# Performance work log

Measured on AMD Instinct MI355X. Metric: run time of the kernel, lower is better.

Reference implementation:

```python
import jax, jax.numpy as jnp
import numpy as np

GS = 256      # grid/node count
PARAM = 128   # feature width
KC = 32       # keepconst (constant features)
I1, I2 = 64, 32
PK = PARAM - KC
K_DIV = 16.0  # neighbor-count normalizer
EPS = 1e-3    # Keras BatchNorm default epsilon
B = 4


def _bn(x, g, b, m, v):
    # inference-mode batch norm over last axis
    return (x - m) * jax.lax.rsqrt(v + EPS) * g + b


def setup_inputs() -> dict:
    key = jax.random.key(0)
    ks = jax.random.split(key, 24)
    mat = (jax.random.uniform(ks[0], (B, GS, GS)) < (K_DIV / GS)).astype(jnp.float32)
    val = jax.random.normal(ks[1], (B, GS, PARAM), dtype=jnp.float32)
    def w(k, shape):
        fan = shape[0] if len(shape) > 1 else shape[0]
        return jax.random.normal(k, shape, dtype=jnp.float32) * (1.0 / np.sqrt(fan))
    inp = {
        'mat': mat, 'val': val,
        'M1': w(ks[2], (2 * PARAM, I1)), 'B1': 0.05 * jax.random.normal(ks[3], (I1,)),
        'M2': w(ks[4], (I1, I2)),        'B2': 0.05 * jax.random.normal(ks[5], (I2,)),
        'M3': w(ks[6], (I2, PK)),        'B3': 0.05 * jax.random.normal(ks[7], (PK,)),
    }
    for idx, d in zip((1, 2, 3), (I1, I2, PK)):
        kk = jax.random.split(ks[7 + idx], 4)
        inp[f'g{idx}'] = 1.0 + 0.1 * jax.random.normal(kk[0], (d,), dtype=jnp.float32)
        inp[f'b{idx}'] = 0.1 * jax.random.normal(kk[1], (d,), dtype=jnp.float32)
        inp[f'm{idx}'] = 0.1 * jax.random.normal(kk[2], (d,), dtype=jnp.float32)
        inp[f'v{idx}'] = jax.random.uniform(kk[3], (d,), dtype=jnp.float32, minval=0.5, maxval=1.5)
    return inp


def reference(mat, val, M1, B1, M2, B2, M3, B3,
              g1, b1, m1, v1, g2, b2, m2, v2, g3, b3, m3, v3):
    con = val[:, :, :KC]
    # selector matmuls == gather: pair i -> (a=i//GS, b=i%GS)
    feat = jnp.repeat(val, GS, axis=1)          # (B, GS*GS, PARAM) = val_a
    vb = jnp.tile(val, (1, GS, 1))              # (B, GS*GS, PARAM) = val_b
    premlp = jnp.concatenate([feat, vb - feat], axis=-1)  # (B, GS*GS, 2*PARAM)
    s = jax.nn.relu(_bn(premlp @ M1 + B1, g1, b1, m1, v1))
    s = jax.nn.relu(_bn(s @ M2 + B2, g2, b2, m2, v2))
    s = jax.nn.relu(_bn(s @ M3 + B3, g3, b3, m3, v3))      # (B, GS*GS, PK)
    res = s.reshape(val.shape[0], GS, GS, PK)               # (B, a, b, PK)
    # masked scatter-sum over neighbor axis b
    summ = jnp.einsum('babk,bab->bak'.replace('a', 'x').replace('b', 'y', 1), res, mat) if False else \
        jnp.einsum('bxyk,bxy->bxk', res, mat)               # (B, GS, PK)
    var = jnp.clip(summ / K_DIV, -1.0, 1.0)                 # advrelu([-1,1]) == clip
    return jnp.concatenate([con, var], axis=-1)             # (B, GS, PARAM)
```

## Files before the change

kernel.cpp:

```cpp
#include <hip/hip_runtime.h>

#define GS    256
#define PARAM 128
#define KC    32
#define I1    64
#define I2    32
#define PK    96
#define B_    4
#define NROWS (B_ * GS)
#define EPS   1e-3f
#define KDIV_INV (1.0f / 16.0f)

constexpr int U_OFF   = 0;
constexpr int W_OFF   = NROWS * I1;
constexpr int M2F_OFF = 2 * NROWS * I1;
constexpr int C2_OFF  = M2F_OFF + I1 * I2;
constexpr int M3F_OFF = C2_OFF + I2;
constexpr int C3_OFF  = M3F_OFF + I2 * PK;
constexpr int C1_OFF  = C3_OFF + PK;

__device__ __forceinline__ float rdlane(float v, int l) {
    return __uint_as_float(__builtin_amdgcn_readlane(__float_as_uint(v), l));
}

__global__ __launch_bounds__(256) void glmlp_precompute(
    const float* __restrict__ val, const float* __restrict__ M1,
    const float* __restrict__ B1,
    const float* __restrict__ M2, const float* __restrict__ B2,
    const float* __restrict__ M3, const float* __restrict__ B3,
    const float* __restrict__ g1, const float* __restrict__ b1,
    const float* __restrict__ m1, const float* __restrict__ v1,
    const float* __restrict__ g2, const float* __restrict__ b2,
    const float* __restrict__ m2, const float* __restrict__ v2,
    const float* __restrict__ g3, const float* __restrict__ b3,
    const float* __restrict__ m3, const float* __restrict__ v3,
    float* __restrict__ ws, float* __restrict__ out)
{
    const int blk = blockIdx.x;
    const int t = threadIdx.x;

    if (blk < NROWS) {
        __shared__ float vrow[PARAM];
        __shared__ float red[4][I1];
        const int r = blk;
        if (t < PARAM) vrow[t] = val[r * PARAM + t];
        if (t < KC) out[r * PARAM + t] = val[r * PARAM + t];
        __syncthreads();

        const int i = t & (I1 - 1);
        const int q = t >> 6;
        const float* __restrict__ Mb = M1 + ((q >> 1) ? (PARAM * I1) : 0);
        const int p0 = (q & 1) * 64;
        float aa = 0.f, bb = 0.f;
        #pragma unroll 8
        for (int p = 0; p < 64; p += 2) {
            aa = fmaf(vrow[p0 + p],     Mb[(p0 + p) * I1 + i],     aa);
            bb = fmaf(vrow[p0 + p + 1], Mb[(p0 + p + 1) * I1 + i], bb);
        }
        red[q][i] = aa + bb;
        __syncthreads();

        if (q == 0) {
            const float T  = red[0][i] + red[1][i];
            const float Wv = red[2][i] + red[3][i];
            const float s1 = g1[i] * rsqrtf(v1[i] + EPS);
            ws[U_OFF + r * I1 + i] = (T - Wv) * s1;
            ws[W_OFF + r * I1 + i] = Wv * s1;
        }
    } else {
        if (t < I1) {
            const float s1 = g1[t] * rsqrtf(v1[t] + EPS);
            ws[C1_OFF + t] = B1[t] * s1 + b1[t] - m1[t] * s1;
        }
        if (t < I2) {
            const float s2 = g2[t] * rsqrtf(v2[t] + EPS);
            ws[C2_OFF + t] = B2[t] * s2 + b2[t] - m2[t] * s2;
        }
        if (t < PK) {
            const float s3 = g3[t] * rsqrtf(v3[t] + EPS);
            ws[C3_OFF + t] = B3[t] * s3 + b3[t] - m3[t] * s3;
        }
        for (int idx = t; idx < I1 * I2; idx += 256) {
            const int j = idx & (I2 - 1);
            const float s2 = g2[j] * rsqrtf(v2[j] + EPS);
            ws[M2F_OFF + idx] = M2[idx] * s2;
        }
        for (int idx = t; idx < I2 * PK; idx += 256) {
            const int k = idx % PK;
            const float s3 = g3[k] * rsqrtf(v3[k] + EPS);
            ws[M3F_OFF + idx] = M3[idx] * s3;
        }
    }
}

__global__ __launch_bounds__(256) void glmlp_pairs(
    const float* __restrict__ mat, const float* __restrict__ ws,
    float* __restrict__ out)
{
    const int t = threadIdx.x;
    const int lane = t & 63;
    const int r = blockIdx.x * 4 + (t >> 6);
    const int jj = lane & 31;
    const int wbase = r & ~(GS - 1);
    const float* __restrict__ W = ws + W_OFF;

    const unsigned long long bal0 = __ballot(mat[r * GS +   0 + lane] != 0.f);
    const unsigned long long bal1 = __ballot(mat[r * GS +  64 + lane] != 0.f);
    const unsigned long long bal2 = __ballot(mat[r * GS + 128 + lane] != 0.f);
    const unsigned long long bal3 = __ballot(mat[r * GS + 192 + lane] != 0.f);

    float m2col[I1];
    #pragma unroll
    for (int s = 0; s < I1; ++s)
        m2col[s] = ws[M2F_OFF + s * I2 + jj];
    float m3a[I2], m3b[I2];
    #pragma unroll
    for (int i = 0; i < I2; ++i) {
        m3a[i] = ws[M3F_OFF + i * PK + lane];
        m3b[i] = ws[M3F_OFF + i * PK + 64 + jj];
    }
    const float ux  = ws[U_OFF + r * I1 + lane] + ws[C1_OFF + lane];
    const float c2j = ws[C2_OFF + jj];
    const float c30 = ws[C3_OFF + lane];
    const float c31 = ws[C3_OFF + 64 + jj];

    unsigned long long cur = bal0;
    int c = 0;
    auto advance = [&]() -> int {
        while (cur == 0ULL) {
            ++c;
            if (c == 1)      cur = bal1;
            else if (c == 2) cur = bal2;
            else if (c == 3) cur = bal3;
            else             return -1;
        }
        const int b = __builtin_ctzll(cur);
        cur &= cur - 1;
        return (c << 6) + b;
    };

    float acc0 = 0.f, acc1 = 0.f;

    int y = advance();
    float wv = (y >= 0) ? W[(wbase + y) * I1 + lane] : 0.f;
    while (y >= 0) {
        const int yn = advance();
        const float wvn = (yn >= 0) ? W[(wbase + yn) * I1 + lane] : 0.f;

        const float h1 = fmaxf(ux + wv, 0.f);

        float a0 = 0.f, a1 = 0.f, a2 = 0.f, a3 = 0.f;
        #pragma unroll
        for (int s = 0; s < I1; s += 4) {
            a0 = fmaf(rdlane(h1, s + 0), m2col[s + 0], a0);
            a1 = fmaf(rdlane(h1, s + 1), m2col[s + 1], a1);
            a2 = fmaf(rdlane(h1, s + 2), m2col[s + 2], a2);
            a3 = fmaf(rdlane(h1, s + 3), m2col[s + 3], a3);
        }
        const float h2 = fmaxf((a0 + a1) + (a2 + a3) + c2j, 0.f);

        float d0a = c30, d0b = 0.f, d1a = c31, d1b = 0.f;
        #pragma unroll
        for (int i = 0; i < I2; i += 2) {
            const float he = rdlane(h2, i);
            const float ho = rdlane(h2, i + 1);
            d0a = fmaf(he, m3a[i],     d0a);
            d0b = fmaf(ho, m3a[i + 1], d0b);
            d1a = fmaf(he, m3b[i],     d1a);
            d1b = fmaf(ho, m3b[i + 1], d1b);
        }
        acc0 += fmaxf(d0a + d0b, 0.f);
        acc1 += fmaxf(d1a + d1b, 0.f);

        y = yn;
        wv = wvn;
    }

    {
        const float v0 = fminf(fmaxf(acc0 * KDIV_INV, -1.f), 1.f);
        out[r * PARAM + KC + lane] = v0;
        if (lane < 32) {
            const float v1 = fminf(fmaxf(acc1 * KDIV_INV, -1.f), 1.f);
            out[r * PARAM + KC + 64 + lane] = v1;
        }
    }
}

extern "C" void kernel_launch(void* const* d_in, const int* in_sizes, int n_in,
                              void* d_out, int out_size, void* d_ws, size_t ws_size,
                              hipStream_t stream) {
    const float* mat = (const float*)d_in[0];
    const float* val = (const float*)d_in[1];
    const float* M1  = (const float*)d_in[2];
    const float* B1  = (const float*)d_in[3];
    const float* M2  = (const float*)d_in[4];
    const float* B2  = (const float*)d_in[5];
    const float* M3  = (const float*)d_in[6];
    const float* B3  = (const float*)d_in[7];
    const float* g1  = (const float*)d_in[8];
    const float* b1  = (const float*)d_in[9];
    const float* m1  = (const float*)d_in[10];
    const float* v1  = (const float*)d_in[11];
    const float* g2  = (const float*)d_in[12];
    const float* b2  = (const float*)d_in[13];
    const float* m2  = (const float*)d_in[14];
    const float* v2  = (const float*)d_in[15];
    const float* g3  = (const float*)d_in[16];
    const float* b3  = (const float*)d_in[17];
    const float* m3  = (const float*)d_in[18];
    const float* v3  = (const float*)d_in[19];

    float* ws  = (float*)d_ws;
    float* out = (float*)d_out;

    hipLaunchKernelGGL(glmlp_precompute, dim3(NROWS + 1), dim3(256), 0, stream,
                       val, M1, B1, M2, B2, M3, B3,
                       g1, b1, m1, v1, g2, b2, m2, v2, g3, b3, m3, v3,
                       ws, out);

    hipLaunchKernelGGL(glmlp_pairs, dim3(NROWS / 4), dim3(256), 0, stream,
                       mat, ws, out);
}
```

Before: 122.5 us.

## Split each row's neighbors across four waves and fold BN constants into pairs kernel

The pairs kernel now assigns one block per row and has its four wavefronts stride through the row's neighbor list, then reduces their partial sums in shared memory. Previously each wave handled a whole row on its own, with 256 blocks. This raises parallelism from 256 to 1024 blocks, at the cost of a shared-memory reduction and a barrier. The folded BN weights and biases for layers 2 and 3 are now computed inside every block instead of in an extra precompute block, which adds redundant per-block loads and rsqrt work.

```diff
diff --git a/kernel.cpp b/kernel.cpp
--- a/kernel.cpp
+++ b/kernel.cpp
@@ -11,13 +11,8 @@
 #define EPS   1e-3f
 #define KDIV_INV (1.0f / 16.0f)
 
-constexpr int U_OFF   = 0;
-constexpr int W_OFF   = NROWS * I1;
-constexpr int M2F_OFF = 2 * NROWS * I1;
-constexpr int C2_OFF  = M2F_OFF + I1 * I2;
-constexpr int M3F_OFF = C2_OFF + I2;
-constexpr int C3_OFF  = M3F_OFF + I2 * PK;
-constexpr int C1_OFF  = C3_OFF + PK;
+constexpr int U_OFF = 0;
+constexpr int W_OFF = NROWS * I1;
 
 __device__ __forceinline__ float rdlane(float v, int l) {
     return __uint_as_float(__builtin_amdgcn_readlane(__float_as_uint(v), l));
@@ -25,81 +20,59 @@
 
 __global__ __launch_bounds__(256) void glmlp_precompute(
     const float* __restrict__ val, const float* __restrict__ M1,
-    const float* __restrict__ B1,
+    const float* __restrict__ g1, const float* __restrict__ v1,
+    float* __restrict__ ws, float* __restrict__ out)
+{
+    __shared__ float vrow[PARAM];
+    __shared__ float red[4][I1];
+    const int r = blockIdx.x;
+    const int t = threadIdx.x;
+
+    if (t < PARAM) vrow[t] = val[r * PARAM + t];
+    if (t < KC) out[r * PARAM + t] = val[r * PARAM + t];
+    __syncthreads();
+
+    const int i = t & (I1 - 1);
+    const int q = t >> 6;
+    const float* __restrict__ Mb = M1 + ((q >> 1) ? (PARAM * I1) : 0);
+    const int p0 = (q & 1) * 64;
+    float aa = 0.f, bb = 0.f;
+    #pragma unroll 8
+    for (int p = 0; p < 64; p += 2) {
+        aa = fmaf(vrow[p0 + p],     Mb[(p0 + p) * I1 + i],     aa);
+        bb = fmaf(vrow[p0 + p + 1], Mb[(p0 + p + 1) * I1 + i], bb);
+    }
+    red[q][i] = aa + bb;
+    __syncthreads();
+
+    if (q == 0) {
+        const float T  = red[0][i] + red[1][i];
+        const float Wv = red[2][i] + red[3][i];
+        const float s1 = g1[i] * rsqrtf(v1[i] + EPS);
+        ws[U_OFF + r * I1 + i] = (T - Wv) * s1;
+        ws[W_OFF + r * I1 + i] = Wv * s1;
+    }
+}
+
+__global__ __launch_bounds__(256) void glmlp_pairs(
+    const float* __restrict__ mat, const float* __restrict__ ws,
     const float* __restrict__ M2, const float* __restrict__ B2,
     const float* __restrict__ M3, const float* __restrict__ B3,
-    const float* __restrict__ g1, const float* __restrict__ b1,
-    const float* __restrict__ m1, const float* __restrict__ v1,
+    const float* __restrict__ B1, const float* __restrict__ g1,
+    const float* __restrict__ b1, const float* __restrict__ m1,
+    const float* __restrict__ v1,
     const float* __restrict__ g2, const float* __restrict__ b2,
     const float* __restrict__ m2, const float* __restrict__ v2,
     const float* __restrict__ g3, const float* __restrict__ b3,
     const float* __restrict__ m3, const float* __restrict__ v3,
-    float* __restrict__ ws, float* __restrict__ out)
-{
-    const int blk = blockIdx.x;
-    const int t = threadIdx.x;
-
-    if (blk < NROWS) {
-        __shared__ float vrow[PARAM];
-        __shared__ float red[4][I1];
-        const int r = blk;
-        if (t < PARAM) vrow[t] = val[r * PARAM + t];
-        if (t < KC) out[r * PARAM + t] = val[r * PARAM + t];
-        __syncthreads();
-
-        const int i = t & (I1 - 1);
-        const int q = t >> 6;
-        const float* __restrict__ Mb = M1 + ((q >> 1) ? (PARAM * I1) : 0);
-        const int p0 = (q & 1) * 64;
-        float aa = 0.f, bb = 0.f;
-        #pragma unroll 8
-        for (int p = 0; p < 64; p += 2) {
-            aa = fmaf(vrow[p0 + p],     Mb[(p0 + p) * I1 + i],     aa);
-            bb = fmaf(vrow[p0 + p + 1], Mb[(p0 + p + 1) * I1 + i], bb);
-        }
-        red[q][i] = aa + bb;
-        __syncthreads();
-
-        if (q == 0) {
-            const float T  = red[0][i] + red[1][i];
-            const float Wv = red[2][i] + red[3][i];
-            const float s1 = g1[i] * rsqrtf(v1[i] + EPS);
-            ws[U_OFF + r * I1 + i] = (T - Wv) * s1;
-            ws[W_OFF + r * I1 + i] = Wv * s1;
-        }
-    } else {
-        if (t < I1) {
-            const float s1 = g1[t] * rsqrtf(v1[t] + EPS);
-            ws[C1_OFF + t] = B1[t] * s1 + b1[t] - m1[t] * s1;
-        }
-        if (t < I2) {
-            const float s2 = g2[t] * rsqrtf(v2[t] + EPS);
-            ws[C2_OFF + t] = B2[t] * s2 + b2[t] - m2[t] * s2;
-        }
-        if (t < PK) {
-            const float s3 = g3[t] * rsqrtf(v3[t] + EPS);
-            ws[C3_OFF + t] = B3[t] * s3 + b3[t] - m3[t] * s3;
-        }
-        for (int idx = t; idx < I1 * I2; idx += 256) {
-            const int j = idx & (I2 - 1);
-            const float s2 = g2[j] * rsqrtf(v2[j] + EPS);
-            ws[M2F_OFF + idx] = M2[idx] * s2;
-        }
-        for (int idx = t; idx < I2 * PK; idx += 256) {
-            const int k = idx % PK;
-            const float s3 = g3[k] * rsqrtf(v3[k] + EPS);
-            ws[M3F_OFF + idx] = M3[idx] * s3;
-        }
-    }
-}
-
-__global__ __launch_bounds__(256) void glmlp_pairs(
-    const float* __restrict__ mat, const float* __restrict__ ws,
     float* __restrict__ out)
 {
+    __shared__ float partial[4][PK];
+
     const int t = threadIdx.x;
     const int lane = t & 63;
-    const int r = blockIdx.x * 4 + (t >> 6);
+    const int w = t >> 6;
+    const int r = blockIdx.x;
     const int jj = lane & 31;
     const int wbase = r & ~(GS - 1);
     const float* __restrict__ W = ws + W_OFF;
@@ -109,20 +82,27 @@
     const unsigned long long bal2 = __ballot(mat[r * GS + 128 + lane] != 0.f);
     const unsigned long long bal3 = __ballot(mat[r * GS + 192 + lane] != 0.f);
 
+    const float s2j = g2[jj] * rsqrtf(v2[jj] + EPS);
     float m2col[I1];
     #pragma unroll
     for (int s = 0; s < I1; ++s)
-        m2col[s] = ws[M2F_OFF + s * I2 + jj];
+        m2col[s] = M2[s * I2 + jj] * s2j;
+    const float c2j = (B2[jj] - m2[jj]) * s2j + b2[jj];
+
+    const float s3l = g3[lane] * rsqrtf(v3[lane] + EPS);
+    const float s3h = g3[64 + jj] * rsqrtf(v3[64 + jj] + EPS);
     float m3a[I2], m3b[I2];
     #pragma unroll
     for (int i = 0; i < I2; ++i) {
-        m3a[i] = ws[M3F_OFF + i * PK + lane];
-        m3b[i] = ws[M3F_OFF + i * PK + 64 + jj];
-    }
-    const float ux  = ws[U_OFF + r * I1 + lane] + ws[C1_OFF + lane];
-    const float c2j = ws[C2_OFF + jj];
-    const float c30 = ws[C3_OFF + lane];
-    const float c31 = ws[C3_OFF + 64 + jj];
+        m3a[i] = M3[i * PK + lane] * s3l;
+        m3b[i] = M3[i * PK + 64 + jj] * s3h;
+    }
+    const float c30 = (B3[lane] - m3[lane]) * s3l + b3[lane];
+    const float c31 = (B3[64 + jj] - m3[64 + jj]) * s3h + b3[64 + jj];
+
+    const float s1l = g1[lane] * rsqrtf(v1[lane] + EPS);
+    const float c1l = (B1[lane] - m1[lane]) * s1l + b1[lane];
+    const float ux  = ws[U_OFF + r * I1 + lane] + c1l;
 
     unsigned long long cur = bal0;
     int c = 0;
@@ -142,9 +122,11 @@
     float acc0 = 0.f, acc1 = 0.f;
 
     int y = advance();
+    for (int s = 0; s < w && y >= 0; ++s) y = advance();
     float wv = (y >= 0) ? W[(wbase + y) * I1 + lane] : 0.f;
     while (y >= 0) {
-        const int yn = advance();
+        int yn = advance();
+        for (int s = 0; s < 3 && yn >= 0; ++s) yn = advance();
         const float wvn = (yn >= 0) ? W[(wbase + yn) * I1 + lane] : 0.f;
 
         const float h1 = fmaxf(ux + wv, 0.f);
@@ -176,13 +158,15 @@
         wv = wvn;
     }
 
-    {
-        const float v0 = fminf(fmaxf(acc0 * KDIV_INV, -1.f), 1.f);
-        out[r * PARAM + KC + lane] = v0;
-        if (lane < 32) {
-            const float v1 = fminf(fmaxf(acc1 * KDIV_INV, -1.f), 1.f);
-            out[r * PARAM + KC + 64 + lane] = v1;
-        }
+    partial[w][lane] = acc0;
+    if (lane < 32) partial[w][64 + lane] = acc1;
+    __syncthreads();
+
+    if (t < PK) {
+        float v = (partial[0][t] + partial[1][t] + partial[2][t] + partial[3][t])
+                  * KDIV_INV;
+        v = fminf(fmaxf(v, -1.0f), 1.0f);
+        out[r * PARAM + KC + t] = v;
     }
 }
 
@@ -213,11 +197,11 @@
     float* ws  = (float*)d_ws;
     float* out = (float*)d_out;
 
-    hipLaunchKernelGGL(glmlp_precompute, dim3(NROWS + 1), dim3(256), 0, stream,
-                       val, M1, B1, M2, B2, M3, B3,
-                       g1, b1, m1, v1, g2, b2, m2, v2, g3, b3, m3, v3,
-                       ws, out);
-
-    hipLaunchKernelGGL(glmlp_pairs, dim3(NROWS / 4), dim3(256), 0, stream,
-                       mat, ws, out);
-}
+    hipLaunchKernelGGL(glmlp_precompute, dim3(NROWS), dim3(256), 0, stream,
+                       val, M1, g1, v1, ws, out);
+
+    hipLaunchKernelGGL(glmlp_pairs, dim3(NROWS), dim3(256), 0, stream,
+                       mat, ws, M2, B2, M3, B3,
+                       B1, g1, b1, m1, v1, g2, b2, m2, v2, g3, b3, m3, v3,
+                       out);
+}
```

Measured after the change: 111.3 us. 1.1x faster.
